# Performance work log

Hardware: AMD Instinct MI355X
Metric: run time of the kernel (lower is better)

Reference implementation:

```python
import jax, jax.numpy as jnp
import numpy as np

B, C, H, W = 16, 512, 64, 64


def setup_inputs() -> dict:
    key = jax.random.key(0)
    k1, k2 = jax.random.split(key)
    img_feat = jax.random.normal(k1, (B, C, H, W), dtype=jnp.float32)
    text_feat = jax.random.normal(k2, (B, C, H, W), dtype=jnp.float32)
    gamma = jnp.zeros((1,), dtype=jnp.float32)
    return {"img_feat": img_feat, "text_feat": text_feat, "gamma": gamma}


def reference(img_feat, text_feat, gamma):
    b, c, h, w = img_feat.shape
    q = img_feat.reshape(b, c, h * w)          # [B, C, HW]
    kv = text_feat.reshape(b, c, h * w)        # [B, C, HW]
    # channel-attention map: [B, C, C]
    attn = jnp.einsum('bcn,bdn->bcd', q, kv)
    attn = jax.nn.softmax(attn, axis=-1)
    info = jnp.einsum('bcd,bdn->bcn', attn, kv).reshape(b, c, h, w)
    return gamma * info + img_feat
```

## Files before the change

kernel.cpp:

```cpp
#include <hip/hip_runtime.h>
#include <hip/hip_bf16.h>


constexpr int NB = 16;
constexpr int NC = 512;
constexpr int NHW = 4096;
constexpr int SPLITK = 4;

typedef float f32x4 __attribute__((ext_vector_type(4)));
typedef __bf16 bf16x4 __attribute__((ext_vector_type(4)));
typedef __bf16 bf16x8 __attribute__((ext_vector_type(8)));

template <int STAGEF32, int EPI, int MDIM, int NDIM, int KDIM, int SPLITS>
__global__ __launch_bounds__(512) void gemm_bt(
    const void* __restrict__ Ap, const void* __restrict__ Bp,
    float* __restrict__ Dp, const float* __restrict__ img,
    const float* __restrict__ gammap, float* __restrict__ outp) {
  __shared__ __bf16 sA[128 * 64];
  __shared__ __bf16 sB[128 * 64];

  const int t = threadIdx.x;
  const int lane = t & 63;
  const int wave = t >> 6;
  const int wr = wave >> 2;
  const int wc = wave & 3;

  const int batch = blockIdx.z / SPLITS;
  const int split = blockIdx.z % SPLITS;

  const long aBatch = (long)batch * MDIM * KDIM;
  const long bBatch = (long)batch * NDIM * KDIM;
  const int aRow0 = blockIdx.x * 128;
  const int bRow0 = blockIdx.y * 128;

  constexpr int KSUB = KDIM / SPLITS;
  const int kBeg = split * KSUB;
  const int kEnd = kBeg + KSUB;

  f32x4 acc[4][2] = {};

  for (int k0 = kBeg; k0 < kEnd; k0 += 64) {
    if constexpr (STAGEF32) {
      const float* A = (const float*)Ap + aBatch;
      const float* Bm = (const float*)Bp + bBatch;
      const int c4 = (t & 15) * 4;
      const int rb = t >> 4;
#pragma unroll
      for (int i = 0; i < 4; ++i) {
        const int r = rb + 32 * i;
        f32x4 va = *(const f32x4*)(A + (long)(aRow0 + r) * KDIM + k0 + c4);
        f32x4 vb = *(const f32x4*)(Bm + (long)(bRow0 + r) * KDIM + k0 + c4);
        const int idx = r * 64 + (c4 ^ ((r & 7) << 3));
        bf16x4 ha = {(__bf16)va.x, (__bf16)va.y, (__bf16)va.z, (__bf16)va.w};
        bf16x4 hb = {(__bf16)vb.x, (__bf16)vb.y, (__bf16)vb.z, (__bf16)vb.w};
        *(bf16x4*)&sA[idx] = ha;
        *(bf16x4*)&sB[idx] = hb;
      }
    } else {
      const __bf16* A = (const __bf16*)Ap + aBatch;
      const __bf16* Bm = (const __bf16*)Bp + bBatch;
      const int c8 = (t & 7) * 8;
      const int rb = t >> 3;
#pragma unroll
      for (int i = 0; i < 2; ++i) {
        const int r = rb + 64 * i;
        bf16x8 va = *(const bf16x8*)(A + (long)(aRow0 + r) * KDIM + k0 + c8);
        bf16x8 vb = *(const bf16x8*)(Bm + (long)(bRow0 + r) * KDIM + k0 + c8);
        const int idx = r * 64 + (c8 ^ ((r & 7) << 3));
        *(bf16x8*)&sA[idx] = va;
        *(bf16x8*)&sB[idx] = vb;
      }
    }
    __syncthreads();

#pragma unroll
    for (int kk = 0; kk < 2; ++kk) {
      const int kb = kk * 32 + ((lane >> 4) << 3);
      bf16x8 af[4], bfr[2];
#pragma unroll
      for (int m = 0; m < 4; ++m) {
        const int r = wr * 64 + m * 16 + (lane & 15);
        af[m] = *(const bf16x8*)&sA[r * 64 + (kb ^ ((r & 7) << 3))];
      }
#pragma unroll
      for (int n = 0; n < 2; ++n) {
        const int r = wc * 32 + n * 16 + (lane & 15);
        bfr[n] = *(const bf16x8*)&sB[r * 64 + (kb ^ ((r & 7) << 3))];
      }
#pragma unroll
      for (int m = 0; m < 4; ++m)
#pragma unroll
        for (int n = 0; n < 2; ++n)
          acc[m][n] = __builtin_amdgcn_mfma_f32_16x16x32_bf16(
              af[m], bfr[n], acc[m][n], 0, 0, 0);
    }
    __syncthreads();
  }

  if constexpr (EPI == 0) {
    float* D = Dp + ((long)split * NB + batch) * MDIM * NDIM;
    const int m0 = aRow0 + wr * 64;
    const int n0 = bRow0 + wc * 32;
#pragma unroll
    for (int m = 0; m < 4; ++m)
#pragma unroll
      for (int n = 0; n < 2; ++n) {
        const int row0 = m0 + m * 16 + ((lane >> 4) << 2);
        const int col = n0 + n * 16 + (lane & 15);
#pragma unroll
        for (int r = 0; r < 4; ++r)
          D[(long)(row0 + r) * NDIM + col] = acc[m][n][r];
      }
  } else {
    const float g = gammap[0];
    const long obase = (long)batch * NC * NHW;
    const int sp0 = aRow0 + wr * 64;
    const int ch0 = bRow0 + wc * 32;
#pragma unroll
    for (int m = 0; m < 4; ++m)
#pragma unroll
      for (int n = 0; n < 2; ++n) {
        const int sp = sp0 + m * 16 + ((lane >> 4) << 2);
        const int ch = ch0 + n * 16 + (lane & 15);
        const long idx = obase + (long)ch * NHW + sp;
        f32x4 iv = *(const f32x4*)(img + idx);
        f32x4 ov;
#pragma unroll
        for (int r = 0; r < 4; ++r) ov[r] = g * acc[m][n][r] + iv[r];
        *(f32x4*)(outp + idx) = ov;
      }
  }
}

__global__ __launch_bounds__(256) void transpose_cast(
    const float* __restrict__ kv, __bf16* __restrict__ kvT) {
  __shared__ __bf16 tile[64 * 68];
  const int t = threadIdx.x;
  const int n0 = blockIdx.x * 64;
  const int d0 = blockIdx.y * 64;
  const long ibase = (long)blockIdx.z * NC * NHW;

  const int nc4 = (t & 15) * 4;
  const int dr0 = t >> 4;
#pragma unroll
  for (int i = 0; i < 4; ++i) {
    const int dr = dr0 + 16 * i;
    f32x4 v = *(const f32x4*)(kv + ibase + (long)(d0 + dr) * NHW + n0 + nc4);
    bf16x4 h = {(__bf16)v.x, (__bf16)v.y, (__bf16)v.z, (__bf16)v.w};
    *(bf16x4*)&tile[dr * 68 + nc4] = h;
  }
  __syncthreads();

  const long obase = (long)blockIdx.z * NHW * NC;
  const int nr = t >> 2;
  const int dc0 = t & 3;
#pragma unroll
  for (int i = 0; i < 2; ++i) {
    const int dc = dc0 + 4 * i;
    bf16x8 pk;
#pragma unroll
    for (int j = 0; j < 8; ++j) pk[j] = tile[(dc * 8 + j) * 68 + nr];
    *(bf16x8*)(kvT + obase + (long)(n0 + nr) * NC + d0 + dc * 8) = pk;
  }
}

__global__ __launch_bounds__(256) void softmax_rows(
    const float* __restrict__ attn, __bf16* __restrict__ P) {
  const int row = blockIdx.x * 4 + (threadIdx.x >> 6);
  const int lane = threadIdx.x & 63;
  const long PS = (long)NB * NC * NC;
  const float* src = attn + (long)row * NC;

  float x[8] = {0.f, 0.f, 0.f, 0.f, 0.f, 0.f, 0.f, 0.f};
#pragma unroll
  for (int s = 0; s < SPLITK; ++s) {
    f32x4 v0 = *(const f32x4*)(src + s * PS + lane * 4);
    f32x4 v1 = *(const f32x4*)(src + s * PS + 256 + lane * 4);
#pragma unroll
    for (int r = 0; r < 4; ++r) { x[r] += v0[r]; x[4 + r] += v1[r]; }
  }

  float mx = x[0];
#pragma unroll
  for (int r = 1; r < 8; ++r) mx = fmaxf(mx, x[r]);
#pragma unroll
  for (int off = 32; off >= 1; off >>= 1) mx = fmaxf(mx, __shfl_xor(mx, off));

  float e[8], s = 0.f;
#pragma unroll
  for (int r = 0; r < 8; ++r) { e[r] = expf(x[r] - mx); s += e[r]; }
#pragma unroll
  for (int off = 32; off >= 1; off >>= 1) s += __shfl_xor(s, off);
  const float inv = 1.0f / s;

  __bf16* dst = P + (long)row * NC;
  bf16x4 h0, h1;
#pragma unroll
  for (int r = 0; r < 4; ++r) {
    h0[r] = (__bf16)(e[r] * inv);
    h1[r] = (__bf16)(e[4 + r] * inv);
  }
  *(bf16x4*)(dst + lane * 4) = h0;
  *(bf16x4*)(dst + 256 + lane * 4) = h1;
}

extern "C" void kernel_launch(void* const* d_in, const int* in_sizes, int n_in,
                              void* d_out, int out_size, void* d_ws,
                              size_t ws_size, hipStream_t stream) {
  const float* img = (const float*)d_in[0];
  const float* txt = (const float*)d_in[1];
  const float* gamma = (const float*)d_in[2];
  float* out = (float*)d_out;

  char* ws = (char*)d_ws;
  float* attnP = (float*)ws;
  __bf16* kvT = (__bf16*)ws;
  __bf16* P = (__bf16*)(ws + (size_t)64 * 1024 * 1024);

  gemm_bt<1, 0, NC, NC, NHW, SPLITK>
      <<<dim3(NC / 128, NC / 128, NB * SPLITK), 512, 0, stream>>>(
          img, txt, attnP, nullptr, nullptr, nullptr);

  softmax_rows<<<dim3(NB * NC / 4), 256, 0, stream>>>(attnP, P);

  transpose_cast<<<dim3(NHW / 64, NC / 64, NB), 256, 0, stream>>>(txt, kvT);

  gemm_bt<0, 1, NHW, NC, NC, 1>
      <<<dim3(NHW / 128, NC / 128, NB), 512, 0, stream>>>(
          kvT, P, nullptr, img, gamma, out);
}
```

Baseline: 258.0 us.

## Pre-cast inputs to bf16, double-buffer GEMM with direct global-to-LDS loads

Adds separate kernels that cast img to bf16 (staged in the output buffer) and cast text to bf16 in both normal and transposed layouts in one pass. The shared GEMM now uses global_load_lds with double-buffered LDS and a waitcnt-based two-stage pipeline, remaps workgroup IDs in XCD-aware order, and sets a launch-bounds occupancy hint. Split-K drops from 4 to 2, or to 1 when the workspace is small, which shrinks the partial-sum buffer and the softmax reduction. The cost is extra full-tensor cast passes and reuse of the output buffer as scratch before the final write.

Result: faster. 242.7 us (-5.9%).

```diff
diff --git a/kernel.cpp b/kernel.cpp
--- a/kernel.cpp
+++ b/kernel.cpp
@@ -5,19 +5,24 @@
 constexpr int NB = 16;
 constexpr int NC = 512;
 constexpr int NHW = 4096;
-constexpr int SPLITK = 4;
 
 typedef float f32x4 __attribute__((ext_vector_type(4)));
 typedef __bf16 bf16x4 __attribute__((ext_vector_type(4)));
 typedef __bf16 bf16x8 __attribute__((ext_vector_type(8)));
 
-template <int STAGEF32, int EPI, int MDIM, int NDIM, int KDIM, int SPLITS>
-__global__ __launch_bounds__(512) void gemm_bt(
-    const void* __restrict__ Ap, const void* __restrict__ Bp,
+__device__ __forceinline__ void gload16(const void* g, void* l) {
+  __builtin_amdgcn_global_load_lds(
+      (const __attribute__((address_space(1))) void*)g,
+      (__attribute__((address_space(3))) void*)l, 16, 0, 0);
+}
+
+template <int EPI, int MDIM, int NDIM, int KDIM, int SPLITS>
+__global__ __launch_bounds__(512, 4) void gemm_bt(
+    const __bf16* __restrict__ A, const __bf16* __restrict__ B,
     float* __restrict__ Dp, const float* __restrict__ img,
     const float* __restrict__ gammap, float* __restrict__ outp) {
-  __shared__ __bf16 sA[128 * 64];
-  __shared__ __bf16 sB[128 * 64];
+  __shared__ __bf16 sA[2][128 * 64];
+  __shared__ __bf16 sB[2][128 * 64];
 
   const int t = threadIdx.x;
   const int lane = t & 63;
@@ -25,54 +30,43 @@
   const int wr = wave >> 2;
   const int wc = wave & 3;
 
-  const int batch = blockIdx.z / SPLITS;
-  const int split = blockIdx.z % SPLITS;
-
-  const long aBatch = (long)batch * MDIM * KDIM;
-  const long bBatch = (long)batch * NDIM * KDIM;
-  const int aRow0 = blockIdx.x * 128;
-  const int bRow0 = blockIdx.y * 128;
-
+  constexpr int GX = MDIM / 128;
+  constexpr int GY = NDIM / 128;
+  constexpr int NWG = GX * GY * NB * SPLITS;
+  constexpr int QX = NWG / 8;
+  int flat = blockIdx.x + GX * (blockIdx.y + GY * blockIdx.z);
+  flat = (flat & 7) * QX + (flat >> 3);
+  const int bx = flat % GX;
+  const int by = (flat / GX) % GY;
+  const int bz = flat / (GX * GY);
+  const int batch = bz / SPLITS;
+  const int split = bz % SPLITS;
+
+  const int aRow0 = bx * 128;
+  const int bRow0 = by * 128;
   constexpr int KSUB = KDIM / SPLITS;
+  constexpr int NT = KSUB / 64;
   const int kBeg = split * KSUB;
-  const int kEnd = kBeg + KSUB;
+
+  const int rl = lane >> 3;
+  const int csrc = ((lane & 7) ^ rl) * 8;
+  const __bf16* Abase = A + (long)batch * MDIM * KDIM +
+                        (long)(aRow0 + wave * 16 + rl) * KDIM + csrc + kBeg;
+  const __bf16* Bbase = B + (long)batch * NDIM * KDIM +
+                        (long)(bRow0 + wave * 16 + rl) * KDIM + csrc + kBeg;
+  const int ldsOff = wave * 16 * 64;
+
+  auto stage = [&](int buf, int kof) {
+#pragma unroll
+    for (int i = 0; i < 2; ++i) {
+      gload16(Abase + kof + (long)i * 8 * KDIM, &sA[buf][ldsOff + i * 8 * 64]);
+      gload16(Bbase + kof + (long)i * 8 * KDIM, &sB[buf][ldsOff + i * 8 * 64]);
+    }
+  };
 
   f32x4 acc[4][2] = {};
 
-  for (int k0 = kBeg; k0 < kEnd; k0 += 64) {
-    if constexpr (STAGEF32) {
-      const float* A = (const float*)Ap + aBatch;
-      const float* Bm = (const float*)Bp + bBatch;
-      const int c4 = (t & 15) * 4;
-      const int rb = t >> 4;
-#pragma unroll
-      for (int i = 0; i < 4; ++i) {
-        const int r = rb + 32 * i;
-        f32x4 va = *(const f32x4*)(A + (long)(aRow0 + r) * KDIM + k0 + c4);
-        f32x4 vb = *(const f32x4*)(Bm + (long)(bRow0 + r) * KDIM + k0 + c4);
-        const int idx = r * 64 + (c4 ^ ((r & 7) << 3));
-        bf16x4 ha = {(__bf16)va.x, (__bf16)va.y, (__bf16)va.z, (__bf16)va.w};
-        bf16x4 hb = {(__bf16)vb.x, (__bf16)vb.y, (__bf16)vb.z, (__bf16)vb.w};
-        *(bf16x4*)&sA[idx] = ha;
-        *(bf16x4*)&sB[idx] = hb;
-      }
-    } else {
-      const __bf16* A = (const __bf16*)Ap + aBatch;
-      const __bf16* Bm = (const __bf16*)Bp + bBatch;
-      const int c8 = (t & 7) * 8;
-      const int rb = t >> 3;
-#pragma unroll
-      for (int i = 0; i < 2; ++i) {
-        const int r = rb + 64 * i;
-        bf16x8 va = *(const bf16x8*)(A + (long)(aRow0 + r) * KDIM + k0 + c8);
-        bf16x8 vb = *(const bf16x8*)(Bm + (long)(bRow0 + r) * KDIM + k0 + c8);
-        const int idx = r * 64 + (c8 ^ ((r & 7) << 3));
-        *(bf16x8*)&sA[idx] = va;
-        *(bf16x8*)&sB[idx] = vb;
-      }
-    }
-    __syncthreads();
-
+  auto compute_tile = [&](int buf) {
 #pragma unroll
     for (int kk = 0; kk < 2; ++kk) {
       const int kb = kk * 32 + ((lane >> 4) << 3);
@@ -80,12 +74,12 @@
 #pragma unroll
       for (int m = 0; m < 4; ++m) {
         const int r = wr * 64 + m * 16 + (lane & 15);
-        af[m] = *(const bf16x8*)&sA[r * 64 + (kb ^ ((r & 7) << 3))];
+        af[m] = *(const bf16x8*)&sA[buf][r * 64 + (kb ^ ((r & 7) << 3))];
       }
 #pragma unroll
       for (int n = 0; n < 2; ++n) {
         const int r = wc * 32 + n * 16 + (lane & 15);
-        bfr[n] = *(const bf16x8*)&sB[r * 64 + (kb ^ ((r & 7) << 3))];
+        bfr[n] = *(const bf16x8*)&sB[buf][r * 64 + (kb ^ ((r & 7) << 3))];
       }
 #pragma unroll
       for (int m = 0; m < 4; ++m)
@@ -94,8 +88,22 @@
           acc[m][n] = __builtin_amdgcn_mfma_f32_16x16x32_bf16(
               af[m], bfr[n], acc[m][n], 0, 0, 0);
     }
-    __syncthreads();
-  }
+  };
+
+  stage(0, 0);
+  int cur = 0;
+#pragma unroll 1
+  for (int tt = 0; tt < NT - 1; ++tt) {
+    stage(cur ^ 1, (tt + 1) * 64);
+    asm volatile("s_waitcnt vmcnt(4)" ::: "memory");
+    __builtin_amdgcn_s_barrier();
+    compute_tile(cur);
+    __builtin_amdgcn_s_barrier();
+    cur ^= 1;
+  }
+  asm volatile("s_waitcnt vmcnt(0)" ::: "memory");
+  __builtin_amdgcn_s_barrier();
+  compute_tile(cur);
 
   if constexpr (EPI == 0) {
     float* D = Dp + ((long)split * NB + batch) * MDIM * NDIM;
@@ -132,8 +140,22 @@
   }
 }
 
-__global__ __launch_bounds__(256) void transpose_cast(
-    const float* __restrict__ kv, __bf16* __restrict__ kvT) {
+__global__ __launch_bounds__(256) void cast_q(const float* __restrict__ src,
+                                              __bf16* __restrict__ dst) {
+  const long N = (long)NB * NC * NHW;
+  const long stride = (long)gridDim.x * 256 * 8;
+  for (long i = ((long)blockIdx.x * 256 + threadIdx.x) * 8; i < N; i += stride) {
+    f32x4 a = *(const f32x4*)(src + i);
+    f32x4 b = *(const f32x4*)(src + i + 4);
+    bf16x8 h = {(__bf16)a.x, (__bf16)a.y, (__bf16)a.z, (__bf16)a.w,
+                (__bf16)b.x, (__bf16)b.y, (__bf16)b.z, (__bf16)b.w};
+    *(bf16x8*)(dst + i) = h;
+  }
+}
+
+__global__ __launch_bounds__(256) void prep_kv(const float* __restrict__ kv,
+                                               __bf16* __restrict__ kv16,
+                                               __bf16* __restrict__ kvT) {
   __shared__ __bf16 tile[64 * 68];
   const int t = threadIdx.x;
   const int n0 = blockIdx.x * 64;
@@ -148,6 +170,7 @@
     f32x4 v = *(const f32x4*)(kv + ibase + (long)(d0 + dr) * NHW + n0 + nc4);
     bf16x4 h = {(__bf16)v.x, (__bf16)v.y, (__bf16)v.z, (__bf16)v.w};
     *(bf16x4*)&tile[dr * 68 + nc4] = h;
+    *(bf16x4*)(kv16 + ibase + (long)(d0 + dr) * NHW + n0 + nc4) = h;
   }
   __syncthreads();
 
@@ -164,6 +187,7 @@
   }
 }
 
+template <int SPLITS>
 __global__ __launch_bounds__(256) void softmax_rows(
     const float* __restrict__ attn, __bf16* __restrict__ P) {
   const int row = blockIdx.x * 4 + (threadIdx.x >> 6);
@@ -173,7 +197,7 @@
 
   float x[8] = {0.f, 0.f, 0.f, 0.f, 0.f, 0.f, 0.f, 0.f};
 #pragma unroll
-  for (int s = 0; s < SPLITK; ++s) {
+  for (int s = 0; s < SPLITS; ++s) {
     f32x4 v0 = *(const f32x4*)(src + s * PS + lane * 4);
     f32x4 v1 = *(const f32x4*)(src + s * PS + 256 + lane * 4);
 #pragma unroll
@@ -212,20 +236,32 @@
   const float* gamma = (const float*)d_in[2];
   float* out = (float*)d_out;
 
+  __bf16* q16 = (__bf16*)d_out;
+  __bf16* kv16 = (__bf16*)d_out + (size_t)NB * NC * NHW;
+
+  const size_t MiB = 1024 * 1024;
   char* ws = (char*)d_ws;
+  const bool big = ws_size >= 104 * MiB;
+
   float* attnP = (float*)ws;
-  __bf16* kvT = (__bf16*)ws;
-  __bf16* P = (__bf16*)(ws + (size_t)64 * 1024 * 1024);
-
-  gemm_bt<1, 0, NC, NC, NHW, SPLITK>
-      <<<dim3(NC / 128, NC / 128, NB * SPLITK), 512, 0, stream>>>(
-          img, txt, attnP, nullptr, nullptr, nullptr);
-
-  softmax_rows<<<dim3(NB * NC / 4), 256, 0, stream>>>(attnP, P);
-
-  transpose_cast<<<dim3(NHW / 64, NC / 64, NB), 256, 0, stream>>>(txt, kvT);
-
-  gemm_bt<0, 1, NHW, NC, NC, 1>
-      <<<dim3(NHW / 128, NC / 128, NB), 512, 0, stream>>>(
-          kvT, P, nullptr, img, gamma, out);
-}
+  __bf16* P = (__bf16*)(ws + (big ? 32 : 16) * MiB);
+  __bf16* kvT = (__bf16*)(ws + (big ? 40 : 24) * MiB);
+
+  cast_q<<<2048, 256, 0, stream>>>(img, q16);
+  prep_kv<<<dim3(NHW / 64, NC / 64, NB), 256, 0, stream>>>(txt, kv16, kvT);
+
+  if (big)
+    gemm_bt<0, NC, NC, NHW, 2><<<dim3(4, 4, NB * 2), 512, 0, stream>>>(
+        q16, kv16, attnP, nullptr, nullptr, nullptr);
+  else
+    gemm_bt<0, NC, NC, NHW, 1><<<dim3(4, 4, NB), 512, 0, stream>>>(
+        q16, kv16, attnP, nullptr, nullptr, nullptr);
+
+  if (big)
+    softmax_rows<2><<<dim3(NB * NC / 4), 256, 0, stream>>>(attnP, P);
+  else
+    softmax_rows<1><<<dim3(NB * NC / 4), 256, 0, stream>>>(attnP, P);
+
+  gemm_bt<1, NHW, NC, NC, 1><<<dim3(NHW / 128, 4, NB), 512, 0, stream>>>(
+      kvT, P, nullptr, img, gamma, out);
+}
```
